# Kernel tuning notes

Measured on AMD Instinct MI355X. Metric: run time of the kernel, lower is better.

Reference implementation:

```python
import jax, jax.numpy as jnp
import numpy as np

W_POINT = 1.0
W_COEFF = 0.5
W_AFFINE = 0.5


def _euler_xyz_to_matrix(angles):
    # angles: [B, 3] Euler angles, XYZ convention: R = Rx @ Ry @ Rz (pytorch3d style)
    ax, ay, az = angles[:, 0], angles[:, 1], angles[:, 2]
    cx, sx = jnp.cos(ax), jnp.sin(ax)
    cy, sy = jnp.cos(ay), jnp.sin(ay)
    cz, sz = jnp.cos(az), jnp.sin(az)
    one = jnp.ones_like(cx)
    zero = jnp.zeros_like(cx)
    Rx = jnp.stack([one, zero, zero,
                    zero, cx, -sx,
                    zero, sx, cx], axis=-1).reshape(-1, 3, 3)
    Ry = jnp.stack([cy, zero, sy,
                    zero, one, zero,
                    -sy, zero, cy], axis=-1).reshape(-1, 3, 3)
    Rz = jnp.stack([cz, -sz, zero,
                    sz, cz, zero,
                    zero, zero, one], axis=-1).reshape(-1, 3, 3)
    return Rx @ Ry @ Rz


def _chamfer(pred, targ):
    # pred: [B,N,3], targ: [B,M,3]; symmetric chamfer of squared distances
    p2 = jnp.sum(pred * pred, axis=-1)        # [B,N]
    t2 = jnp.sum(targ * targ, axis=-1)        # [B,M]
    d2 = p2[:, :, None] + t2[:, None, :] - 2.0 * jnp.einsum('bnd,bmd->bnm', pred, targ)
    d2 = jnp.maximum(d2, 0.0)
    return jnp.mean(jnp.min(d2, axis=2)) + jnp.mean(jnp.min(d2, axis=1))


def setup_inputs() -> dict:
    key = jax.random.key(0)
    ks = jax.random.split(key, 6)
    B, N, M, K = 16, 4096, 4096, 128
    return {
        'pred_shape': jax.random.normal(ks[0], (B, N, 3), dtype=jnp.float32),
        'pred_weights': jax.random.normal(ks[1], (B, K), dtype=jnp.float32),
        'pred_affine': jax.random.uniform(ks[2], (B, 9), dtype=jnp.float32),
        'targ_shape': jax.random.normal(ks[3], (B, M, 3), dtype=jnp.float32),
        'targ_weights': jax.random.normal(ks[4], (B, K), dtype=jnp.float32),
        'targ_affine': jax.random.uniform(ks[5], (B, 9), dtype=jnp.float32),
    }


def reference(pred_shape, pred_weights, pred_affine, targ_shape, targ_weights, targ_affine):
    rot, trans, scale = targ_affine[:, 0:3], targ_affine[:, 3:6], targ_affine[:, 6:9]
    R = _euler_xyz_to_matrix(rot)                                   # [B,3,3]
    # row-vector convention (pytorch3d Transform3d): p' = (p @ R) * s + t
    targ_moving = jnp.einsum('bmd,bde->bme', targ_shape, R) * scale[:, None, :] + trans[:, None, :]
    point_loss = _chamfer(pred_shape, targ_moving)
    coeff_loss = jnp.mean((pred_weights - targ_weights) ** 2)
    affine_loss = jnp.mean((pred_affine - targ_affine) ** 2)
    total = W_POINT * point_loss + W_COEFF * coeff_loss + W_AFFINE * affine_loss
    return total, point_loss, coeff_loss, affine_loss
```

## Files before the change

kernel.cpp:

```cpp
#include <hip/hip_runtime.h>
#include <math.h>

#define BB 16
#define NN 4096
#define KK 128
#define NTILE 8
#define TS (NN / NTILE)
#define NCHUNK 4
#define QPT 4
#define TPB 256
#define W_POINT  1.0f
#define W_COEFF  0.5f
#define W_AFFINE 0.5f

__device__ inline void compute_affine(const float* __restrict__ aff,
                                      float R[9], float sc[3], float tr[3]) {
    float ax = aff[0], ay = aff[1], az = aff[2];
    tr[0] = aff[3]; tr[1] = aff[4]; tr[2] = aff[5];
    sc[0] = aff[6]; sc[1] = aff[7]; sc[2] = aff[8];
    float cx = cosf(ax), sx = sinf(ax);
    float cy = cosf(ay), sy = sinf(ay);
    float cz = cosf(az), sz = sinf(az);
    R[0] = cy * cz;                 R[1] = -cy * sz;                R[2] = sy;
    R[3] = cx * sz + sx * sy * cz;  R[4] = cx * cz - sx * sy * sz;  R[5] = -sx * cy;
    R[6] = sx * sz - cx * sy * cz;  R[7] = sx * cz + cx * sy * sz;  R[8] = cx * cy;
}

__device__ inline void apply_affine(const float R[9], const float sc[3], const float tr[3],
                                    float x, float y, float z,
                                    float& ox, float& oy, float& oz) {
    ox = fmaf(fmaf(x, R[0], fmaf(y, R[3], z * R[6])), sc[0], tr[0]);
    oy = fmaf(fmaf(x, R[1], fmaf(y, R[4], z * R[7])), sc[1], tr[1]);
    oz = fmaf(fmaf(x, R[2], fmaf(y, R[5], z * R[8])), sc[2], tr[2]);
}

__global__ __launch_bounds__(TPB, 4) void chamfer_kernel(
        const float* __restrict__ pred_shape,
        const float* __restrict__ targ_shape,
        const float* __restrict__ targ_affine,
        unsigned int* __restrict__ pmin) {
    __shared__ float4 lds[TS];

    const int bx    = blockIdx.x;
    const int tile  = bx & (NTILE - 1);
    const int chunk = (bx >> 3) & (NCHUNK - 1);
    const int b     = bx >> 5;
    const int dir   = blockIdx.y;
    const int tid   = threadIdx.x;

    float R[9], sc[3], tr[3];
    compute_affine(targ_affine + b * 9, R, sc, tr);

    const int rbase = tile * TS;
    if (dir == 0) {
        const float* ts = targ_shape + ((size_t)b * NN + rbase) * 3;
        for (int i = tid; i < TS; i += TPB) {
            float x = ts[i * 3 + 0], y = ts[i * 3 + 1], z = ts[i * 3 + 2];
            float mx, my, mz;
            apply_affine(R, sc, tr, x, y, z, mx, my, mz);
            lds[i] = make_float4(mx, my, mz, fmaf(mx, mx, fmaf(my, my, mz * mz)));
        }
    } else {
        const float* ps = pred_shape + ((size_t)b * NN + rbase) * 3;
        for (int i = tid; i < TS; i += TPB) {
            float x = ps[i * 3 + 0], y = ps[i * 3 + 1], z = ps[i * 3 + 2];
            lds[i] = make_float4(x, y, z, fmaf(x, x, fmaf(y, y, z * z)));
        }
    }
    __syncthreads();

    const int qbase = chunk * (TPB * QPT);
    float ax[QPT], ay[QPT], az[QPT], q2[QPT], mn[QPT];
    #pragma unroll
    for (int k = 0; k < QPT; ++k) {
        const int qi = qbase + k * TPB + tid;
        float x, y, z;
        if (dir == 0) {
            const float* p = pred_shape + ((size_t)b * NN + qi) * 3;
            x = p[0]; y = p[1]; z = p[2];
        } else {
            const float* t = targ_shape + ((size_t)b * NN + qi) * 3;
            apply_affine(R, sc, tr, t[0], t[1], t[2], x, y, z);
        }
        q2[k] = fmaf(x, x, fmaf(y, y, z * z));
        ax[k] = -2.0f * x; ay[k] = -2.0f * y; az[k] = -2.0f * z;
        mn[k] = 1e30f;
    }

    for (int j = 0; j < TS; j += 4) {
        float4 t0 = lds[j + 0], t1 = lds[j + 1], t2 = lds[j + 2], t3 = lds[j + 3];
        #pragma unroll
        for (int k = 0; k < QPT; ++k) {
            float v0 = fmaf(ax[k], t0.x, fmaf(ay[k], t0.y, fmaf(az[k], t0.z, t0.w)));
            float v1 = fmaf(ax[k], t1.x, fmaf(ay[k], t1.y, fmaf(az[k], t1.z, t1.w)));
            float v2 = fmaf(ax[k], t2.x, fmaf(ay[k], t2.y, fmaf(az[k], t2.z, t2.w)));
            float v3 = fmaf(ax[k], t3.x, fmaf(ay[k], t3.y, fmaf(az[k], t3.z, t3.w)));
            mn[k] = fminf(mn[k], fminf(fminf(v0, v1), fminf(v2, v3)));
        }
    }

    #pragma unroll
    for (int k = 0; k < QPT; ++k) {
        const int qi = qbase + k * TPB + tid;
        float d = fmaxf(q2[k] + mn[k], 0.0f);
        atomicMin(&pmin[((size_t)dir * BB + b) * NN + qi], __float_as_uint(d));
    }
}

__global__ __launch_bounds__(1024) void finalize_kernel(
        const unsigned int* __restrict__ pmin,
        const float* __restrict__ pred_w,  const float* __restrict__ targ_w,
        const float* __restrict__ pred_aff, const float* __restrict__ targ_aff,
        float* __restrict__ out) {
    const int tid = threadIdx.x;

    float ps = 0.0f;
    const int total4 = (2 * BB * NN) / 4;
    const uint4* pm4 = (const uint4*)pmin;
    for (int i = tid; i < total4; i += 1024) {
        uint4 u = pm4[i];
        ps += __uint_as_float(u.x) + __uint_as_float(u.y)
            + __uint_as_float(u.z) + __uint_as_float(u.w);
    }
    float cs = 0.0f;
    for (int i = tid; i < BB * KK; i += 1024) {
        float d = pred_w[i] - targ_w[i];
        cs = fmaf(d, d, cs);
    }
    float as = 0.0f;
    if (tid < BB * 9) {
        float d = pred_aff[tid] - targ_aff[tid];
        as = d * d;
    }

    #pragma unroll
    for (int off = 32; off > 0; off >>= 1) {
        ps += __shfl_down(ps, off);
        cs += __shfl_down(cs, off);
        as += __shfl_down(as, off);
    }
    __shared__ float sps[16], scs[16], sas[16];
    const int wid = tid >> 6;
    if ((tid & 63) == 0) { sps[wid] = ps; scs[wid] = cs; sas[wid] = as; }
    __syncthreads();
    if (tid == 0) {
        float p = 0.0f, c = 0.0f, a = 0.0f;
        #pragma unroll
        for (int w = 0; w < 16; ++w) { p += sps[w]; c += scs[w]; a += sas[w]; }
        float point  = p / (float)(BB * NN);
        float coeff  = c / (float)(BB * KK);
        float affine = a / (float)(BB * 9);
        out[0] = W_POINT * point + W_COEFF * coeff + W_AFFINE * affine;
        out[1] = point;
        out[2] = coeff;
        out[3] = affine;
    }
}

extern "C" void kernel_launch(void* const* d_in, const int* in_sizes, int n_in,
                              void* d_out, int out_size, void* d_ws, size_t ws_size,
                              hipStream_t stream) {
    const float* pred_shape = (const float*)d_in[0];
    const float* pred_w     = (const float*)d_in[1];
    const float* pred_aff   = (const float*)d_in[2];
    const float* targ_shape = (const float*)d_in[3];
    const float* targ_w     = (const float*)d_in[4];
    const float* targ_aff   = (const float*)d_in[5];
    float* out = (float*)d_out;
    unsigned int* pmin = (unsigned int*)d_ws;

    hipMemsetAsync(pmin, 0x7f, (size_t)2 * BB * NN * sizeof(unsigned int), stream);

    chamfer_kernel<<<dim3(BB * NCHUNK * NTILE, 2), TPB, 0, stream>>>(
        pred_shape, targ_shape, targ_aff, pmin);
    finalize_kernel<<<1, 1024, 0, stream>>>(pmin, pred_w, targ_w,
                                            pred_aff, targ_aff, out);
}
```

Before: 123.1 us.

## Retile chamfer to 8 queries per thread and split final reduction

Sets the target tile to 256 points with 16 tiles and 2 chunks, so each thread holds 8 queries and reuses every shared-memory load across twice as many FMAs. Fewer query chunks also mean each point is written by 16 atomicMin operations instead of 8 per tile split. The single-block finalize over 128K values becomes a 32-block partial reduction followed by a small combine kernel. This adds one kernel launch and more register pressure from QPT=8, which could lower occupancy.

```diff
diff --git a/kernel.cpp b/kernel.cpp
--- a/kernel.cpp
+++ b/kernel.cpp
@@ -4,10 +4,10 @@
 #define BB 16
 #define NN 4096
 #define KK 128
-#define NTILE 8
+#define NTILE 16
 #define TS (NN / NTILE)
-#define NCHUNK 4
-#define QPT 4
+#define NCHUNK 2
+#define QPT 8
 #define TPB 256
 #define W_POINT  1.0f
 #define W_COEFF  0.5f
@@ -43,7 +43,7 @@
 
     const int bx    = blockIdx.x;
     const int tile  = bx & (NTILE - 1);
-    const int chunk = (bx >> 3) & (NCHUNK - 1);
+    const int chunk = (bx >> 4) & (NCHUNK - 1);
     const int b     = bx >> 5;
     const int dir   = blockIdx.y;
     const int tid   = threadIdx.x;
@@ -51,20 +51,18 @@
     float R[9], sc[3], tr[3];
     compute_affine(targ_affine + b * 9, R, sc, tr);
 
-    const int rbase = tile * TS;
-    if (dir == 0) {
-        const float* ts = targ_shape + ((size_t)b * NN + rbase) * 3;
-        for (int i = tid; i < TS; i += TPB) {
-            float x = ts[i * 3 + 0], y = ts[i * 3 + 1], z = ts[i * 3 + 2];
+    {
+        const int rbase = tile * TS;
+        if (dir == 0) {
+            const float* ts = targ_shape + ((size_t)b * NN + rbase + tid) * 3;
+            float x = ts[0], y = ts[1], z = ts[2];
             float mx, my, mz;
             apply_affine(R, sc, tr, x, y, z, mx, my, mz);
-            lds[i] = make_float4(mx, my, mz, fmaf(mx, mx, fmaf(my, my, mz * mz)));
-        }
-    } else {
-        const float* ps = pred_shape + ((size_t)b * NN + rbase) * 3;
-        for (int i = tid; i < TS; i += TPB) {
-            float x = ps[i * 3 + 0], y = ps[i * 3 + 1], z = ps[i * 3 + 2];
-            lds[i] = make_float4(x, y, z, fmaf(x, x, fmaf(y, y, z * z)));
+            lds[tid] = make_float4(mx, my, mz, fmaf(mx, mx, fmaf(my, my, mz * mz)));
+        } else {
+            const float* ps = pred_shape + ((size_t)b * NN + rbase + tid) * 3;
+            float x = ps[0], y = ps[1], z = ps[2];
+            lds[tid] = make_float4(x, y, z, fmaf(x, x, fmaf(y, y, z * z)));
         }
     }
     __syncthreads();
@@ -107,24 +105,38 @@
     }
 }
 
-__global__ __launch_bounds__(1024) void finalize_kernel(
+__global__ __launch_bounds__(TPB) void reduce_pmin(
         const unsigned int* __restrict__ pmin,
+        float* __restrict__ partials) {
+    const int tid = threadIdx.x;
+    const uint4* pm4 = (const uint4*)(pmin + (size_t)blockIdx.x * 4096);
+    float ps = 0.0f;
+    #pragma unroll
+    for (int r = 0; r < 4; ++r) {
+        uint4 u = pm4[r * TPB + tid];
+        ps += __uint_as_float(u.x) + __uint_as_float(u.y)
+            + __uint_as_float(u.z) + __uint_as_float(u.w);
+    }
+    #pragma unroll
+    for (int off = 32; off > 0; off >>= 1) ps += __shfl_down(ps, off);
+    __shared__ float sps[4];
+    const int wid = tid >> 6;
+    if ((tid & 63) == 0) sps[wid] = ps;
+    __syncthreads();
+    if (tid == 0) partials[blockIdx.x] = sps[0] + sps[1] + sps[2] + sps[3];
+}
+
+__global__ __launch_bounds__(TPB) void final_combine(
+        const float* __restrict__ partials,
         const float* __restrict__ pred_w,  const float* __restrict__ targ_w,
         const float* __restrict__ pred_aff, const float* __restrict__ targ_aff,
         float* __restrict__ out) {
     const int tid = threadIdx.x;
-
-    float ps = 0.0f;
-    const int total4 = (2 * BB * NN) / 4;
-    const uint4* pm4 = (const uint4*)pmin;
-    for (int i = tid; i < total4; i += 1024) {
-        uint4 u = pm4[i];
-        ps += __uint_as_float(u.x) + __uint_as_float(u.y)
-            + __uint_as_float(u.z) + __uint_as_float(u.w);
-    }
+    float ps = (tid < 32) ? partials[tid] : 0.0f;
     float cs = 0.0f;
-    for (int i = tid; i < BB * KK; i += 1024) {
-        float d = pred_w[i] - targ_w[i];
+    #pragma unroll
+    for (int r = 0; r < (BB * KK) / TPB; ++r) {
+        float d = pred_w[r * TPB + tid] - targ_w[r * TPB + tid];
         cs = fmaf(d, d, cs);
     }
     float as = 0.0f;
@@ -132,21 +144,20 @@
         float d = pred_aff[tid] - targ_aff[tid];
         as = d * d;
     }
-
     #pragma unroll
     for (int off = 32; off > 0; off >>= 1) {
         ps += __shfl_down(ps, off);
         cs += __shfl_down(cs, off);
         as += __shfl_down(as, off);
     }
-    __shared__ float sps[16], scs[16], sas[16];
+    __shared__ float sps[4], scs[4], sas[4];
     const int wid = tid >> 6;
     if ((tid & 63) == 0) { sps[wid] = ps; scs[wid] = cs; sas[wid] = as; }
     __syncthreads();
     if (tid == 0) {
-        float p = 0.0f, c = 0.0f, a = 0.0f;
-        #pragma unroll
-        for (int w = 0; w < 16; ++w) { p += sps[w]; c += scs[w]; a += sas[w]; }
+        float p = sps[0] + sps[1] + sps[2] + sps[3];
+        float c = scs[0] + scs[1] + scs[2] + scs[3];
+        float a = sas[0] + sas[1] + sas[2] + sas[3];
         float point  = p / (float)(BB * NN);
         float coeff  = c / (float)(BB * KK);
         float affine = a / (float)(BB * 9);
@@ -168,11 +179,13 @@
     const float* targ_aff   = (const float*)d_in[5];
     float* out = (float*)d_out;
     unsigned int* pmin = (unsigned int*)d_ws;
+    float* partials = (float*)(pmin + 2 * BB * NN);
 
     hipMemsetAsync(pmin, 0x7f, (size_t)2 * BB * NN * sizeof(unsigned int), stream);
 
     chamfer_kernel<<<dim3(BB * NCHUNK * NTILE, 2), TPB, 0, stream>>>(
         pred_shape, targ_shape, targ_aff, pmin);
-    finalize_kernel<<<1, 1024, 0, stream>>>(pmin, pred_w, targ_w,
-                                            pred_aff, targ_aff, out);
+    reduce_pmin<<<32, TPB, 0, stream>>>(pmin, partials);
+    final_combine<<<1, TPB, 0, stream>>>(partials, pred_w, targ_w,
+                                         pred_aff, targ_aff, out);
 }
```

Result: faster. 112.8 us (-8.4%).
